# Performance work log

Measured on AMD Instinct MI355X. Metric: run time of the kernel, lower is better.

The kernel has to match this reference:

```python
import jax, jax.numpy as jnp
import numpy as np

EMBED_DIM = 2048
NUM_HEADS = 16
HEAD_DIM = EMBED_DIM // NUM_HEADS  # 128
GROUP = 256
NEG = -1e9


def setup_inputs() -> dict:
    key = jax.random.key(0)
    ks = jax.random.split(key, 4)
    B, N, C = 2, 8192, EMBED_DIM
    s = 1.0 / np.sqrt(C).astype(np.float32)
    return {
        "x": jax.random.normal(ks[0], (B, N, C), jnp.float32),
        "Wq": jax.random.normal(ks[1], (C, C), jnp.float32) * s,
        "bq": jnp.zeros((C,), jnp.float32),
        "Wk": jax.random.normal(ks[2], (C, C), jnp.float32) * s,
        "bk": jnp.zeros((C,), jnp.float32),
        "Wv": jax.random.normal(ks[3], (C, C), jnp.float32) * s,
        "bv": jnp.zeros((C,), jnp.float32),
    }


def _s2_attn(x, Wq, bq, Wk, bk, Wv, bv):
    B, N, C = x.shape
    H, hd, gs = NUM_HEADS, HEAD_DIM, GROUP
    G = N // gs
    half = H // 2

    def heads(t):  # [B,N,C] -> [B,H,N,hd]
        return t.reshape(B, N, H, hd).transpose(0, 2, 1, 3)

    q = heads(x @ Wq.T + bq)
    k = heads(x @ Wk.T + bk)
    v = heads(x @ Wv.T + bv)

    def shift(t, s):  # shift second half of heads along sequence
        return jnp.concatenate([t[:, :half], jnp.roll(t[:, half:], s, axis=2)], axis=1)

    q, k, v = shift(q, -(gs // 2)), shift(k, -(gs // 2)), shift(v, -(gs // 2))

    # group-local attention: [B,H,G,gs,hd]
    qg = q.reshape(B, H, G, gs, hd)
    kg = k.reshape(B, H, G, gs, hd)
    vg = v.reshape(B, H, G, gs, hd)

    scores = jnp.einsum("bhgqd,bhgkd->bhgqk", qg, kg) / np.sqrt(hd).astype(x.dtype)
    causal = jnp.triu(jnp.ones((gs, gs), bool), 1)  # mask strictly-upper triangle
    scores = jnp.where(causal, NEG, scores)
    attn = jax.nn.softmax(scores, axis=-1)
    out = jnp.einsum("bhgqk,bhgkd->bhgqd", attn, vg).reshape(B, H, N, hd)

    out = shift(out, gs // 2)  # un-shift the shifted heads
    return out.transpose(0, 2, 1, 3).reshape(B, N, C)


def reference(x, Wq, bq, Wk, bk, Wv, bv):
    return _s2_attn(x, Wq, bq, Wk, bk, Wv, bv)
```

## Files before the change

kernel.cpp:

```cpp
#include <hip/hip_runtime.h>
#include <hip/hip_bf16.h>

#define NSEQ 8192
#define CDIM 2048
#define NHEAD 16
#define HD 128

typedef short short8 __attribute__((ext_vector_type(8)));
typedef short short4v __attribute__((ext_vector_type(4)));
typedef float float4v __attribute__((ext_vector_type(4)));

__device__ __forceinline__ short f2bf(float f) {
    __hip_bfloat16 h = __float2bfloat16(f);
    return *reinterpret_cast<short*>(&h);
}

__device__ __forceinline__ void async_load16(const short* g, short* l) {
    __builtin_amdgcn_global_load_lds((const __attribute__((address_space(1))) void*)g,
                                     (__attribute__((address_space(3))) void*)l,
                                     16, 0, 0);
}

#define X8 (33554432 / 8)
#define W8 (4194304 / 8)

__global__ __launch_bounds__(256) void cvt_all(
    const float* __restrict__ x, const float* __restrict__ wq,
    const float* __restrict__ wk, const float* __restrict__ wv,
    short* __restrict__ xb, short* __restrict__ wqb,
    short* __restrict__ wkb, short* __restrict__ wvb)
{
    const size_t i = (size_t)blockIdx.x * blockDim.x + threadIdx.x;
    const float* src;
    short* dst;
    size_t off;
    if (i < X8)              { src = x;  dst = xb;  off = i; }
    else if (i < X8 + W8)    { src = wq; dst = wqb; off = i - X8; }
    else if (i < X8 + 2*W8)  { src = wk; dst = wkb; off = i - X8 - W8; }
    else                     { src = wv; dst = wvb; off = i - X8 - 2*(size_t)W8; }
    const float4v a = ((const float4v*)src)[off * 2];
    const float4v b = ((const float4v*)src)[off * 2 + 1];
    short8 o;
    for (int j = 0; j < 4; j++) { o[j] = f2bf(a[j]); o[4 + j] = f2bf(b[j]); }
    ((short8*)dst)[off] = o;
}

#define PBAR()  asm volatile("s_barrier" ::: "memory")
#define LGKM0() do { asm volatile("s_waitcnt lgkmcnt(0)" ::: "memory"); \
                     __builtin_amdgcn_sched_barrier(0); } while (0)
#define VMC4()  asm volatile("s_waitcnt vmcnt(4)" ::: "memory")
#define VMC0()  asm volatile("s_waitcnt vmcnt(0)" ::: "memory")

#define MFMA(d, x, y) d = __builtin_amdgcn_mfma_f32_16x16x32_bf16(x, y, d, 0, 0, 0)

__global__ __launch_bounds__(512, 2) void qkv_gemm8(
    const short* __restrict__ xb,
    const short* __restrict__ W, const float* __restrict__ bias,
    float* __restrict__ qout, short* __restrict__ kt, short* __restrict__ vt,
    const int mat)
{
    __shared__ short lds[2][2][256 * 64];

    const int tid  = threadIdx.x;
    const int w    = tid >> 6;
    const int lane = tid & 63;
    const int quad = lane >> 4;
    const int l15  = lane & 15;
    const int wm   = w >> 2;
    const int wn   = w & 3;

    const int id    = (blockIdx.x & 7) * 64 + (blockIdx.x >> 3);
    const int mtile = id >> 3;
    const int ntile = id & 7;
    const int M0 = mtile << 8;
    const int N0 = ntile << 8;

    const short* Ab = xb + (size_t)M0 * CDIM;
    const short* Bb = W  + (size_t)N0 * CDIM;

    const int stg_row = tid >> 3;
    const int stg_col = ((tid & 7) * 8) ^ (((tid >> 3) & 7) << 3);
    const int cswz    = (lane & 7) << 3;

    float bvals[4];
#pragma unroll
    for (int j = 0; j < 4; ++j)
        bvals[j] = bias[N0 + wn * 64 + j * 16 + l15];
    VMC0();

    float4v acc[8][4];
#pragma unroll
    for (int i = 0; i < 8; ++i)
#pragma unroll
        for (int j = 0; j < 4; ++j)
            acc[i][j] = (float4v){0.f, 0.f, 0.f, 0.f};

    auto stage = [&](int bufi, int ab, int h, int t, const short* src) {
        short* l0 = &lds[bufi][ab][h * 8192 + w * 512];
        const short* g = src + (size_t)(h * 128 + stg_row) * CDIM + t * 64 + stg_col;
        async_load16(g, l0);
        async_load16(g + (size_t)64 * CDIM, l0 + 4096);
    };
    auto ldA = [&](int bufi, int i, int ks) -> short8 {
        const int row = wm * 128 + i * 16 + l15;
        return *(const short8*)&lds[bufi][0][row * 64 + ((ks * 32 + quad * 8) ^ cswz)];
    };
    auto ldB = [&](int bufi, int j, int ks) -> short8 {
        const int row = wn * 64 + j * 16 + l15;
        return *(const short8*)&lds[bufi][1][row * 64 + ((ks * 32 + quad * 8) ^ cswz)];
    };

    stage(0, 0, 0, 0, Ab); stage(0, 0, 1, 0, Ab);
    stage(0, 1, 0, 0, Bb); stage(0, 1, 1, 0, Bb);
    stage(1, 1, 0, 1, Bb); stage(1, 1, 1, 1, Bb);
    VMC4();
    PBAR();

    short8 a[4][2], b[4][2];
    for (int it = 0; it < 16; ++it) {
        const int t1 = 2 * it + 1;
        const int t2 = (2 * it + 2 > 31) ? 31 : 2 * it + 2;
        const int t3 = (2 * it + 3 > 31) ? 31 : 2 * it + 3;

#pragma unroll
        for (int i = 0; i < 4; ++i) { a[i][0] = ldA(0, i, 0); a[i][1] = ldA(0, i, 1); }
#pragma unroll
        for (int j = 0; j < 2; ++j) { b[j][0] = ldB(0, j, 0); b[j][1] = ldB(0, j, 1); }
        stage(1, 0, 0, t1, Ab); stage(1, 0, 1, t1, Ab);
        PBAR(); LGKM0();
        __builtin_amdgcn_s_setprio(1);
#pragma unroll
        for (int i = 0; i < 4; ++i)
#pragma unroll
            for (int j = 0; j < 2; ++j) { MFMA(acc[i][j], a[i][0], b[j][0]);
                                          MFMA(acc[i][j], a[i][1], b[j][1]); }
        __builtin_amdgcn_s_setprio(0);
        PBAR();

#pragma unroll
        for (int j = 2; j < 4; ++j) { b[j][0] = ldB(0, j, 0); b[j][1] = ldB(0, j, 1); }
        PBAR(); LGKM0();
        __builtin_amdgcn_s_setprio(1);
#pragma unroll
        for (int i = 0; i < 4; ++i)
#pragma unroll
            for (int j = 2; j < 4; ++j) { MFMA(acc[i][j], a[i][0], b[j][0]);
                                          MFMA(acc[i][j], a[i][1], b[j][1]); }
        __builtin_amdgcn_s_setprio(0);
        PBAR();

#pragma unroll
        for (int i = 0; i < 4; ++i) { a[i][0] = ldA(0, 4 + i, 0); a[i][1] = ldA(0, 4 + i, 1); }
        stage(0, 1, 0, t2, Bb);
        PBAR(); LGKM0();
        __builtin_amdgcn_s_setprio(1);
#pragma unroll
        for (int i = 0; i < 4; ++i)
#pragma unroll
            for (int j = 2; j < 4; ++j) { MFMA(acc[4 + i][j], a[i][0], b[j][0]);
                                          MFMA(acc[4 + i][j], a[i][1], b[j][1]); }
        __builtin_amdgcn_s_setprio(0);
        PBAR();

        stage(0, 1, 1, t2, Bb);
        PBAR(); LGKM0();
        __builtin_amdgcn_s_setprio(1);
#pragma unroll
        for (int i = 0; i < 4; ++i)
#pragma unroll
            for (int j = 0; j < 2; ++j) { MFMA(acc[4 + i][j], a[i][0], b[j][0]);
                                          MFMA(acc[4 + i][j], a[i][1], b[j][1]); }
        __builtin_amdgcn_s_setprio(0);
        VMC4();
        PBAR();

#pragma unroll
        for (int i = 0; i < 4; ++i) { a[i][0] = ldA(1, i, 0); a[i][1] = ldA(1, i, 1); }
#pragma unroll
        for (int j = 0; j < 2; ++j) { b[j][0] = ldB(1, j, 0); b[j][1] = ldB(1, j, 1); }
        stage(0, 0, 0, t2, Ab); stage(0, 0, 1, t2, Ab);
        PBAR(); LGKM0();
        __builtin_amdgcn_s_setprio(1);
#pragma unroll
        for (int i = 0; i < 4; ++i)
#pragma unroll
            for (int j = 0; j < 2; ++j) { MFMA(acc[i][j], a[i][0], b[j][0]);
                                          MFMA(acc[i][j], a[i][1], b[j][1]); }
        __builtin_amdgcn_s_setprio(0);
        PBAR();

#pragma unroll
        for (int j = 2; j < 4; ++j) { b[j][0] = ldB(1, j, 0); b[j][1] = ldB(1, j, 1); }
        PBAR(); LGKM0();
        __builtin_amdgcn_s_setprio(1);
#pragma unroll
        for (int i = 0; i < 4; ++i)
#pragma unroll
            for (int j = 2; j < 4; ++j) { MFMA(acc[i][j], a[i][0], b[j][0]);
                                          MFMA(acc[i][j], a[i][1], b[j][1]); }
        __builtin_amdgcn_s_setprio(0);
        PBAR();

#pragma unroll
        for (int i = 0; i < 4; ++i) { a[i][0] = ldA(1, 4 + i, 0); a[i][1] = ldA(1, 4 + i, 1); }
        stage(1, 1, 0, t3, Bb);
        PBAR(); LGKM0();
        __builtin_amdgcn_s_setprio(1);
#pragma unroll
        for (int i = 0; i < 4; ++i)
#pragma unroll
            for (int j = 2; j < 4; ++j) { MFMA(acc[4 + i][j], a[i][0], b[j][0]);
                                          MFMA(acc[4 + i][j], a[i][1], b[j][1]); }
        __builtin_amdgcn_s_setprio(0);
        PBAR();

        stage(1, 1, 1, t3, Bb);
        PBAR(); LGKM0();
        __builtin_amdgcn_s_setprio(1);
#pragma unroll
        for (int i = 0; i < 4; ++i)
#pragma unroll
            for (int j = 0; j < 2; ++j) { MFMA(acc[4 + i][j], a[i][0], b[j][0]);
                                          MFMA(acc[4 + i][j], a[i][1], b[j][1]); }
        __builtin_amdgcn_s_setprio(0);
        VMC4();
        PBAR();
    }

#pragma unroll
    for (int j = 0; j < 4; ++j) {
        const int n = N0 + wn * 64 + j * 16 + l15;
        if (mat == 0) {
#pragma unroll
            for (int i = 0; i < 8; ++i) {
                const int mrow = M0 + wm * 128 + i * 16 + quad * 4;
#pragma unroll
                for (int r = 0; r < 4; ++r)
                    qout[((size_t)(mrow + r) << 11) + n] = acc[i][j][r] + bvals[j];
            }
        } else if (mat == 1) {
            const int h = n >> 7;
            const int d = n & (HD - 1);
#pragma unroll
            for (int i = 0; i < 8; ++i) {
                const int mrow = M0 + wm * 128 + i * 16 + quad * 4;
#pragma unroll
                for (int r = 0; r < 4; ++r) {
                    const int m  = mrow + r;
                    const int bb = m >> 13;
                    const int sq = m & (NSEQ - 1);
                    kt[(((size_t)(bb * NHEAD + h) * NSEQ + sq) << 7) + d] =
                        f2bf(acc[i][j][r] + bvals[j]);
                }
            }
        } else {
            const int h = n >> 7;
            const int d = n & (HD - 1);
#pragma unroll
            for (int i = 0; i < 8; ++i) {
                const int mrow = M0 + wm * 128 + i * 16 + quad * 4;
                const int bb = mrow >> 13;
                const int sq = mrow & (NSEQ - 1);
                short4v o4;
#pragma unroll
                for (int r = 0; r < 4; ++r) o4[r] = f2bf(acc[i][j][r] + bvals[j]);
                *(short4v*)&vt[(((size_t)(bb * NHEAD + h) * HD + d) << 13) + sq] = o4;
            }
        }
    }
}

__global__ __launch_bounds__(512, 1) void s2_attn(const float* qsrc,
                                                  const short* __restrict__ kt,
                                                  const short* __restrict__ vt,
                                                  float* out)
{
    __shared__ short Ks[64 * 136];
    __shared__ short Vt[2][128 * 64];
    __shared__ short Ps[8][32 * 40];

    const int bx = blockIdx.x;
    const int g  = bx & 31;
    const int h  = (bx >> 5) & 15;
    const int b  = bx >> 9;
    const int shift = (h >= 8) ? 128 : 0;
    const int sbase = g * 256 + shift;

    const int tid  = threadIdx.x;
    const int wave = tid >> 6;
    const int lane = tid & 63;
    const int quad = lane >> 4;
    const int l15  = lane & 15;

    const size_t bh = ((size_t)b * NHEAD + h) * NSEQ;
    const short* kg = kt + bh * HD;
    const short* vg = vt + bh * HD;

    const int mtA = wave;
    const int mtB = wave + 8;

    const int vrow_in_w = lane >> 3;
    const int vgcol     = ((lane & 7) * 8) ^ (vrow_in_w << 3);
    const int krow0 = tid >> 4;
    const int kcolb = (tid & 15) * 8;

    short8 kr0, kr1;

    {
        const int p = (sbase + vgcol) & (NSEQ - 1);
#pragma unroll
        for (int c = 0; c < 2; c++) {
            const int d = c * 64 + wave * 8 + vrow_in_w;
            async_load16(vg + (size_t)d * NSEQ + p, &Vt[0][(c * 64 + wave * 8) * 64]);
        }
        const int p0 = (sbase + krow0) & (NSEQ - 1);
        const int p1 = (sbase + krow0 + 32) & (NSEQ - 1);
        kr0 = *(const short8*)(kg + (size_t)p0 * HD + kcolb);
        kr1 = *(const short8*)(kg + (size_t)p1 * HD + kcolb);
    }

    short8 qf[2][4];
#pragma unroll
    for (int im = 0; im < 2; im++) {
        const int mt  = im ? mtB : mtA;
        const int row = mt * 16 + l15;
        const int p   = (sbase + row) & (NSEQ - 1);
        const float* qr = qsrc + (((size_t)(b * NSEQ + p)) << 11) + h * HD;
#pragma unroll
        for (int ks = 0; ks < 4; ks++) {
            const float4v qa = *(const float4v*)(qr + ks * 32 + quad * 8);
            const float4v qb = *(const float4v*)(qr + ks * 32 + quad * 8 + 4);
            short8 f;
#pragma unroll
            for (int j = 0; j < 4; j++) { f[j] = f2bf(qa[j]); f[4 + j] = f2bf(qb[j]); }
            qf[im][ks] = f;
        }
    }

    const float4v fzero = {0.f, 0.f, 0.f, 0.f};
    float4v o[2][8];
#pragma unroll
    for (int im = 0; im < 2; im++)
#pragma unroll
        for (int dt = 0; dt < 8; dt++)
            o[im][dt] = fzero;
    float rs[2][4] = {{0.f, 0.f, 0.f, 0.f}, {0.f, 0.f, 0.f, 0.f}};

    for (int kc = 0; kc < 4; kc++) {
        VMC0();
        *(short8*)&Ks[krow0 * 136 + kcolb]        = kr0;
        *(short8*)&Ks[(krow0 + 32) * 136 + kcolb] = kr1;
        LGKM0();
        PBAR();

        if (kc < 3) {
            const int p = (sbase + (kc + 1) * 64 + vgcol) & (NSEQ - 1);
#pragma unroll
            for (int c = 0; c < 2; c++) {
                const int d = c * 64 + wave * 8 + vrow_in_w;
                async_load16(vg + (size_t)d * NSEQ + p,
                             &Vt[(kc + 1) & 1][(c * 64 + wave * 8) * 64]);
            }
            const int p0 = (sbase + (kc + 1) * 64 + krow0) & (NSEQ - 1);
            const int p1 = (sbase + (kc + 1) * 64 + krow0 + 32) & (NSEQ - 1);
            kr0 = *(const short8*)(kg + (size_t)p0 * HD + kcolb);
            kr1 = *(const short8*)(kg + (size_t)p1 * HD + kcolb);
        }

        const bool hA[2] = {(4 * kc)     <= mtA, (4 * kc + 2) <= mtA};
        const bool hB[2] = {(4 * kc)     <= mtB, (4 * kc + 2) <= mtB};

        float4v s[2][4];
#pragma unroll
        for (int im = 0; im < 2; im++)
#pragma unroll
            for (int nn = 0; nn < 4; nn++)
                s[im][nn] = fzero;
        __builtin_amdgcn_s_setprio(1);
#pragma unroll
        for (int nn = 0; nn < 4; nn++) {
            const int hh = nn >> 1;
            if (hB[hh]) {
                short8 kf[4];
#pragma unroll
                for (int ks = 0; ks < 4; ks++)
                    kf[ks] = *(const short8*)&Ks[(nn * 16 + l15) * 136 + ks * 32 + quad * 8];
                if (hA[hh]) {
#pragma unroll
                    for (int ks = 0; ks < 4; ks++)
                        s[0][nn] = __builtin_amdgcn_mfma_f32_16x16x32_bf16(
                            qf[0][ks], kf[ks], s[0][nn], 0, 0, 0);
                }
#pragma unroll
                for (int ks = 0; ks < 4; ks++)
                    s[1][nn] = __builtin_amdgcn_mfma_f32_16x16x32_bf16(
                        qf[1][ks], kf[ks], s[1][nn], 0, 0, 0);
            }
        }
        __builtin_amdgcn_s_setprio(0);

#pragma unroll
        for (int half = 0; half < 2; half++) {
            if (!hB[half]) continue;
#pragma unroll
            for (int im = 0; im < 2; im++) {
                if (im == 0 && !hA[half]) continue;
                const int mt   = im ? mtB : mtA;
                const int qpos = mt * 16 + quad * 4;
#pragma unroll
                for (int nn2 = 0; nn2 < 2; nn2++) {
                    const int nn   = half * 2 + nn2;
                    const int kpos = kc * 64 + nn * 16 + l15;
#pragma unroll
                    for (int r = 0; r < 4; r++) {
                        const float sv = s[im][nn][r] * 0.088388347648318447f;
                        const float pv = (kpos > qpos + r)
                                             ? 0.f
                                             : __expf(fminf(sv, 30.f));
                        rs[im][r] += pv;
                        Ps[wave][(im * 16 + quad * 4 + r) * 40 + nn2 * 16 + l15] = f2bf(pv);
                    }
                }
            }
            LGKM0();
            short8 pf[2];
            if (hA[half])
                pf[0] = *(const short8*)&Ps[wave][(0 * 16 + l15) * 40 + quad * 8];
            pf[1] = *(const short8*)&Ps[wave][(1 * 16 + l15) * 40 + quad * 8];
            __builtin_amdgcn_s_setprio(1);
#pragma unroll
            for (int dt = 0; dt < 8; dt++) {
                const int d = dt * 16 + l15;
                const short8 vf = *(const short8*)
                    &Vt[kc & 1][d * 64 + ((half * 32 + quad * 8) ^ ((l15 & 7) << 3))];
                if (hA[half])
                    o[0][dt] = __builtin_amdgcn_mfma_f32_16x16x32_bf16(
                        pf[0], vf, o[0][dt], 0, 0, 0);
                o[1][dt] = __builtin_amdgcn_mfma_f32_16x16x32_bf16(
                    pf[1], vf, o[1][dt], 0, 0, 0);
            }
            __builtin_amdgcn_s_setprio(0);
        }
        PBAR();
    }

#pragma unroll
    for (int im = 0; im < 2; im++)
#pragma unroll
        for (int r = 0; r < 4; r++) {
            float v = rs[im][r];
            v += __shfl_xor(v, 1);
            v += __shfl_xor(v, 2);
            v += __shfl_xor(v, 4);
            v += __shfl_xor(v, 8);
            rs[im][r] = v;
        }

#pragma unroll
    for (int im = 0; im < 2; im++) {
        const int mt = im ? mtB : mtA;
#pragma unroll
        for (int r = 0; r < 4; r++) {
            const int row = mt * 16 + quad * 4 + r;
            const int p   = (sbase + row) & (NSEQ - 1);
            const float inv = 1.f / rs[im][r];
            const size_t obase = (((size_t)(b * NSEQ + p)) << 11) + h * HD;
#pragma unroll
            for (int dt = 0; dt < 8; dt++)
                out[obase + dt * 16 + l15] = o[im][dt][r] * inv;
        }
    }
}

extern "C" void kernel_launch(void* const* d_in, const int* in_sizes, int n_in,
                              void* d_out, int out_size, void* d_ws, size_t ws_size,
                              hipStream_t stream) {
    (void)in_sizes; (void)n_in; (void)out_size; (void)ws_size;
    const float* x  = (const float*)d_in[0];
    const float* Wq = (const float*)d_in[1];
    const float* bq = (const float*)d_in[2];
    const float* Wk = (const float*)d_in[3];
    const float* bk = (const float*)d_in[4];
    const float* Wv = (const float*)d_in[5];
    const float* bv = (const float*)d_in[6];

    short* xb  = (short*)d_ws;
    short* wqb = xb  + (size_t)33554432;
    short* wkb = wqb + (size_t)4194304;
    short* wvb = wkb + (size_t)4194304;
    short* kt  = wvb + (size_t)4194304;
    short* vt  = kt  + (size_t)33554432;

    float* outp = (float*)d_out;

    cvt_all<<<dim3(22528), 256, 0, stream>>>(x, Wq, Wk, Wv, xb, wqb, wkb, wvb);
    qkv_gemm8<<<dim3(512), 512, 0, stream>>>(xb, wqb, bq, outp, kt, vt, 0);
    qkv_gemm8<<<dim3(512), 512, 0, stream>>>(xb, wkb, bk, outp, kt, vt, 1);
    qkv_gemm8<<<dim3(512), 512, 0, stream>>>(xb, wvb, bv, outp, kt, vt, 2);
    s2_attn<<<dim3(1024), 512, 0, stream>>>(outp, kt, vt, outp);
}
```

Baseline: 746.6 us.

## Merge Q/K/V GEMM launches into one grid and grid-stride the conversion kernel

The three separate QKV projection GEMM launches become a single 1536-block launch. Each block picks its matrix (Q, K or V) from the block index, with a swizzle that groups the three projections of the same x row tile together to improve L2 reuse of x. This removes two kernel launch gaps and the tail imbalance between them. The fp32-to-bf16 conversion kernel now uses a grid-stride loop with 16 elements per thread and a smaller grid, which cuts block scheduling overhead.

```diff
diff --git a/kernel.cpp b/kernel.cpp
--- a/kernel.cpp
+++ b/kernel.cpp
@@ -21,8 +21,9 @@
                                      16, 0, 0);
 }
 
-#define X8 (33554432 / 8)
-#define W8 (4194304 / 8)
+#define X16 (33554432 / 16)
+#define W16 (4194304 / 16)
+#define TOT16 (X16 + 3 * W16)
 
 __global__ __launch_bounds__(256) void cvt_all(
     const float* __restrict__ x, const float* __restrict__ wq,
@@ -30,19 +31,30 @@
     short* __restrict__ xb, short* __restrict__ wqb,
     short* __restrict__ wkb, short* __restrict__ wvb)
 {
-    const size_t i = (size_t)blockIdx.x * blockDim.x + threadIdx.x;
-    const float* src;
-    short* dst;
-    size_t off;
-    if (i < X8)              { src = x;  dst = xb;  off = i; }
-    else if (i < X8 + W8)    { src = wq; dst = wqb; off = i - X8; }
-    else if (i < X8 + 2*W8)  { src = wk; dst = wkb; off = i - X8 - W8; }
-    else                     { src = wv; dst = wvb; off = i - X8 - 2*(size_t)W8; }
-    const float4v a = ((const float4v*)src)[off * 2];
-    const float4v b = ((const float4v*)src)[off * 2 + 1];
-    short8 o;
-    for (int j = 0; j < 4; j++) { o[j] = f2bf(a[j]); o[4 + j] = f2bf(b[j]); }
-    ((short8*)dst)[off] = o;
+    const size_t stride = (size_t)gridDim.x * blockDim.x;
+    for (size_t i = (size_t)blockIdx.x * blockDim.x + threadIdx.x;
+         i < (size_t)TOT16; i += stride) {
+        const float* src;
+        short* dst;
+        size_t off;
+        if (i < X16)                 { src = x;  dst = xb;  off = i; }
+        else if (i < X16 + W16)      { src = wq; dst = wqb; off = i - X16; }
+        else if (i < X16 + 2 * W16)  { src = wk; dst = wkb; off = i - X16 - W16; }
+        else                         { src = wv; dst = wvb; off = i - X16 - 2 * (size_t)W16; }
+        const float4v* s4 = (const float4v*)src + off * 4;
+        const float4v a0 = s4[0], a1 = s4[1], a2 = s4[2], a3 = s4[3];
+        short8 o0, o1;
+#pragma unroll
+        for (int j = 0; j < 4; j++) {
+            o0[j]     = f2bf(a0[j]);
+            o0[4 + j] = f2bf(a1[j]);
+            o1[j]     = f2bf(a2[j]);
+            o1[4 + j] = f2bf(a3[j]);
+        }
+        short8* d8 = (short8*)dst + off * 2;
+        d8[0] = o0;
+        d8[1] = o1;
+    }
 }
 
 #define PBAR()  asm volatile("s_barrier" ::: "memory")
@@ -55,9 +67,10 @@
 
 __global__ __launch_bounds__(512, 2) void qkv_gemm8(
     const short* __restrict__ xb,
-    const short* __restrict__ W, const float* __restrict__ bias,
-    float* __restrict__ qout, short* __restrict__ kt, short* __restrict__ vt,
-    const int mat)
+    const short* __restrict__ Wq, const float* __restrict__ bq,
+    const short* __restrict__ Wk, const float* __restrict__ bk,
+    const short* __restrict__ Wv, const float* __restrict__ bv,
+    float* __restrict__ qout, short* __restrict__ kt, short* __restrict__ vt)
 {
     __shared__ short lds[2][2][256 * 64];
 
@@ -69,12 +82,16 @@
     const int wm   = w >> 2;
     const int wn   = w & 3;
 
-    const int id    = (blockIdx.x & 7) * 64 + (blockIdx.x >> 3);
-    const int mtile = id >> 3;
-    const int ntile = id & 7;
+    const int id    = (blockIdx.x & 7) * 192 + (blockIdx.x >> 3);
+    const int mtile = id / 24;
+    const int rest  = id - mtile * 24;
+    const int mat   = rest >> 3;
+    const int ntile = rest & 7;
     const int M0 = mtile << 8;
     const int N0 = ntile << 8;
 
+    const short* W    = (mat == 0) ? Wq : (mat == 1) ? Wk : Wv;
+    const float* bias = (mat == 0) ? bq : (mat == 1) ? bk : bv;
     const short* Ab = xb + (size_t)M0 * CDIM;
     const short* Bb = W  + (size_t)N0 * CDIM;
 
@@ -493,9 +510,8 @@
 
     float* outp = (float*)d_out;
 
-    cvt_all<<<dim3(22528), 256, 0, stream>>>(x, Wq, Wk, Wv, xb, wqb, wkb, wvb);
-    qkv_gemm8<<<dim3(512), 512, 0, stream>>>(xb, wqb, bq, outp, kt, vt, 0);
-    qkv_gemm8<<<dim3(512), 512, 0, stream>>>(xb, wkb, bk, outp, kt, vt, 1);
-    qkv_gemm8<<<dim3(512), 512, 0, stream>>>(xb, wvb, bv, outp, kt, vt, 2);
+    cvt_all<<<dim3(2048), 256, 0, stream>>>(x, Wq, Wk, Wv, xb, wqb, wkb, wvb);
+    qkv_gemm8<<<dim3(1536), 512, 0, stream>>>(xb, wqb, bq, wkb, bk, wvb, bv,
+                                              outp, kt, vt);
     s2_attn<<<dim3(1024), 512, 0, stream>>>(outp, kt, vt, outp);
 }
```

After: 726.5 us. -2.7%, faster.

## Merge Q/K/V GEMMs into one persistent kernel with next-tile prefetch

Applied to the files above, without the earlier changes.

Replaces three separate GEMM launches of 512 blocks with one launch of 256 persistent blocks. Each block works through 6 output tiles drawn from the Q, K and V matrices, ordered so tiles that share the same x rows stay on the same XCD. While the epilogue stores the current tile, the block already issues async LDS loads for the next tile, which hides pipeline fill and removes two launch gaps. The trade-off is one resident block per CU instead of two, which lowers the wave-level latency hiding within the main loop.

```diff
diff --git a/kernel.cpp b/kernel.cpp
--- a/kernel.cpp
+++ b/kernel.cpp
@@ -55,9 +55,10 @@
 
 __global__ __launch_bounds__(512, 2) void qkv_gemm8(
     const short* __restrict__ xb,
-    const short* __restrict__ W, const float* __restrict__ bias,
-    float* __restrict__ qout, short* __restrict__ kt, short* __restrict__ vt,
-    const int mat)
+    const short* __restrict__ Wq, const float* __restrict__ bq,
+    const short* __restrict__ Wk, const float* __restrict__ bk,
+    const short* __restrict__ Wv, const float* __restrict__ bv,
+    float* __restrict__ qout, short* __restrict__ kt, short* __restrict__ vt)
 {
     __shared__ short lds[2][2][256 * 64];
 
@@ -69,31 +70,27 @@
     const int wm   = w >> 2;
     const int wn   = w & 3;
 
-    const int id    = (blockIdx.x & 7) * 64 + (blockIdx.x >> 3);
-    const int mtile = id >> 3;
-    const int ntile = id & 7;
-    const int M0 = mtile << 8;
-    const int N0 = ntile << 8;
-
-    const short* Ab = xb + (size_t)M0 * CDIM;
-    const short* Bb = W  + (size_t)N0 * CDIM;
+    const int xcd = blockIdx.x & 7;
+    const int c   = blockIdx.x >> 3;
 
     const int stg_row = tid >> 3;
     const int stg_col = ((tid & 7) * 8) ^ (((tid >> 3) & 7) << 3);
     const int cswz    = (lane & 7) << 3;
 
-    float bvals[4];
-#pragma unroll
-    for (int j = 0; j < 4; ++j)
-        bvals[j] = bias[N0 + wn * 64 + j * 16 + l15];
-    VMC0();
-
-    float4v acc[8][4];
-#pragma unroll
-    for (int i = 0; i < 8; ++i)
-#pragma unroll
-        for (int j = 0; j < 4; ++j)
-            acc[i][j] = (float4v){0.f, 0.f, 0.f, 0.f};
+    auto decode = [&](int a, int& mat, int& M0, int& N0,
+                      const short*& Ab, const short*& Bb, const float*& bias) {
+        const int id    = xcd * 192 + c * 6 + a;
+        const int mtile = id / 24;
+        const int rest  = id - mtile * 24;
+        mat = rest >> 3;
+        const int ntile = rest & 7;
+        M0 = mtile << 8;
+        N0 = ntile << 8;
+        const short* W = (mat == 0) ? Wq : (mat == 1) ? Wk : Wv;
+        bias = (mat == 0) ? bq : (mat == 1) ? bk : bv;
+        Ab = xb + (size_t)M0 * CDIM;
+        Bb = W  + (size_t)N0 * CDIM;
+    };
 
     auto stage = [&](int bufi, int ab, int h, int t, const short* src) {
         short* l0 = &lds[bufi][ab][h * 8192 + w * 512];
@@ -110,162 +107,203 @@
         return *(const short8*)&lds[bufi][1][row * 64 + ((ks * 32 + quad * 8) ^ cswz)];
     };
 
+    int mat, M0, N0;
+    const short *Ab, *Bb;
+    const float* bias;
+    decode(0, mat, M0, N0, Ab, Bb, bias);
+
+    float bvals[4];
+#pragma unroll
+    for (int j = 0; j < 4; ++j)
+        bvals[j] = bias[N0 + wn * 64 + j * 16 + l15];
+
     stage(0, 0, 0, 0, Ab); stage(0, 0, 1, 0, Ab);
     stage(0, 1, 0, 0, Bb); stage(0, 1, 1, 0, Bb);
     stage(1, 1, 0, 1, Bb); stage(1, 1, 1, 1, Bb);
     VMC4();
     PBAR();
 
+    float4v acc[8][4];
     short8 a[4][2], b[4][2];
-    for (int it = 0; it < 16; ++it) {
-        const int t1 = 2 * it + 1;
-        const int t2 = (2 * it + 2 > 31) ? 31 : 2 * it + 2;
-        const int t3 = (2 * it + 3 > 31) ? 31 : 2 * it + 3;
-
-#pragma unroll
-        for (int i = 0; i < 4; ++i) { a[i][0] = ldA(0, i, 0); a[i][1] = ldA(0, i, 1); }
-#pragma unroll
-        for (int j = 0; j < 2; ++j) { b[j][0] = ldB(0, j, 0); b[j][1] = ldB(0, j, 1); }
-        stage(1, 0, 0, t1, Ab); stage(1, 0, 1, t1, Ab);
-        PBAR(); LGKM0();
-        __builtin_amdgcn_s_setprio(1);
-#pragma unroll
-        for (int i = 0; i < 4; ++i)
-#pragma unroll
-            for (int j = 0; j < 2; ++j) { MFMA(acc[i][j], a[i][0], b[j][0]);
-                                          MFMA(acc[i][j], a[i][1], b[j][1]); }
-        __builtin_amdgcn_s_setprio(0);
-        PBAR();
-
-#pragma unroll
-        for (int j = 2; j < 4; ++j) { b[j][0] = ldB(0, j, 0); b[j][1] = ldB(0, j, 1); }
-        PBAR(); LGKM0();
-        __builtin_amdgcn_s_setprio(1);
-#pragma unroll
-        for (int i = 0; i < 4; ++i)
-#pragma unroll
-            for (int j = 2; j < 4; ++j) { MFMA(acc[i][j], a[i][0], b[j][0]);
-                                          MFMA(acc[i][j], a[i][1], b[j][1]); }
-        __builtin_amdgcn_s_setprio(0);
-        PBAR();
-
-#pragma unroll
-        for (int i = 0; i < 4; ++i) { a[i][0] = ldA(0, 4 + i, 0); a[i][1] = ldA(0, 4 + i, 1); }
-        stage(0, 1, 0, t2, Bb);
-        PBAR(); LGKM0();
-        __builtin_amdgcn_s_setprio(1);
-#pragma unroll
-        for (int i = 0; i < 4; ++i)
-#pragma unroll
-            for (int j = 2; j < 4; ++j) { MFMA(acc[4 + i][j], a[i][0], b[j][0]);
-                                          MFMA(acc[4 + i][j], a[i][1], b[j][1]); }
-        __builtin_amdgcn_s_setprio(0);
-        PBAR();
-
-        stage(0, 1, 1, t2, Bb);
-        PBAR(); LGKM0();
-        __builtin_amdgcn_s_setprio(1);
-#pragma unroll
-        for (int i = 0; i < 4; ++i)
-#pragma unroll
-            for (int j = 0; j < 2; ++j) { MFMA(acc[4 + i][j], a[i][0], b[j][0]);
-                                          MFMA(acc[4 + i][j], a[i][1], b[j][1]); }
-        __builtin_amdgcn_s_setprio(0);
-        VMC4();
-        PBAR();
-
-#pragma unroll
-        for (int i = 0; i < 4; ++i) { a[i][0] = ldA(1, i, 0); a[i][1] = ldA(1, i, 1); }
-#pragma unroll
-        for (int j = 0; j < 2; ++j) { b[j][0] = ldB(1, j, 0); b[j][1] = ldB(1, j, 1); }
-        stage(0, 0, 0, t2, Ab); stage(0, 0, 1, t2, Ab);
-        PBAR(); LGKM0();
-        __builtin_amdgcn_s_setprio(1);
-#pragma unroll
-        for (int i = 0; i < 4; ++i)
-#pragma unroll
-            for (int j = 0; j < 2; ++j) { MFMA(acc[i][j], a[i][0], b[j][0]);
-                                          MFMA(acc[i][j], a[i][1], b[j][1]); }
-        __builtin_amdgcn_s_setprio(0);
-        PBAR();
-
-#pragma unroll
-        for (int j = 2; j < 4; ++j) { b[j][0] = ldB(1, j, 0); b[j][1] = ldB(1, j, 1); }
-        PBAR(); LGKM0();
-        __builtin_amdgcn_s_setprio(1);
-#pragma unroll
-        for (int i = 0; i < 4; ++i)
-#pragma unroll
-            for (int j = 2; j < 4; ++j) { MFMA(acc[i][j], a[i][0], b[j][0]);
-                                          MFMA(acc[i][j], a[i][1], b[j][1]); }
-        __builtin_amdgcn_s_setprio(0);
-        PBAR();
-
-#pragma unroll
-        for (int i = 0; i < 4; ++i) { a[i][0] = ldA(1, 4 + i, 0); a[i][1] = ldA(1, 4 + i, 1); }
-        stage(1, 1, 0, t3, Bb);
-        PBAR(); LGKM0();
-        __builtin_amdgcn_s_setprio(1);
-#pragma unroll
-        for (int i = 0; i < 4; ++i)
-#pragma unroll
-            for (int j = 2; j < 4; ++j) { MFMA(acc[4 + i][j], a[i][0], b[j][0]);
-                                          MFMA(acc[4 + i][j], a[i][1], b[j][1]); }
-        __builtin_amdgcn_s_setprio(0);
-        PBAR();
-
-        stage(1, 1, 1, t3, Bb);
-        PBAR(); LGKM0();
-        __builtin_amdgcn_s_setprio(1);
-#pragma unroll
-        for (int i = 0; i < 4; ++i)
-#pragma unroll
-            for (int j = 0; j < 2; ++j) { MFMA(acc[4 + i][j], a[i][0], b[j][0]);
-                                          MFMA(acc[4 + i][j], a[i][1], b[j][1]); }
-        __builtin_amdgcn_s_setprio(0);
-        VMC4();
-        PBAR();
-    }
-
-#pragma unroll
-    for (int j = 0; j < 4; ++j) {
-        const int n = N0 + wn * 64 + j * 16 + l15;
-        if (mat == 0) {
-#pragma unroll
-            for (int i = 0; i < 8; ++i) {
-                const int mrow = M0 + wm * 128 + i * 16 + quad * 4;
-#pragma unroll
-                for (int r = 0; r < 4; ++r)
-                    qout[((size_t)(mrow + r) << 11) + n] = acc[i][j][r] + bvals[j];
-            }
-        } else if (mat == 1) {
-            const int h = n >> 7;
-            const int d = n & (HD - 1);
-#pragma unroll
-            for (int i = 0; i < 8; ++i) {
-                const int mrow = M0 + wm * 128 + i * 16 + quad * 4;
-#pragma unroll
-                for (int r = 0; r < 4; ++r) {
-                    const int m  = mrow + r;
-                    const int bb = m >> 13;
-                    const int sq = m & (NSEQ - 1);
-                    kt[(((size_t)(bb * NHEAD + h) * NSEQ + sq) << 7) + d] =
-                        f2bf(acc[i][j][r] + bvals[j]);
+
+    for (int asg = 0; asg < 6; ++asg) {
+#pragma unroll
+        for (int i = 0; i < 8; ++i)
+#pragma unroll
+            for (int j = 0; j < 4; ++j)
+                acc[i][j] = (float4v){0.f, 0.f, 0.f, 0.f};
+
+        for (int it = 0; it < 16; ++it) {
+            const int t1 = 2 * it + 1;
+            const int t2 = (2 * it + 2 > 31) ? 31 : 2 * it + 2;
+            const int t3 = (2 * it + 3 > 31) ? 31 : 2 * it + 3;
+
+#pragma unroll
+            for (int i = 0; i < 4; ++i) { a[i][0] = ldA(0, i, 0); a[i][1] = ldA(0, i, 1); }
+#pragma unroll
+            for (int j = 0; j < 2; ++j) { b[j][0] = ldB(0, j, 0); b[j][1] = ldB(0, j, 1); }
+            stage(1, 0, 0, t1, Ab); stage(1, 0, 1, t1, Ab);
+            PBAR(); LGKM0();
+            __builtin_amdgcn_s_setprio(1);
+#pragma unroll
+            for (int i = 0; i < 4; ++i)
+#pragma unroll
+                for (int j = 0; j < 2; ++j) { MFMA(acc[i][j], a[i][0], b[j][0]);
+                                              MFMA(acc[i][j], a[i][1], b[j][1]); }
+            __builtin_amdgcn_s_setprio(0);
+            PBAR();
+
+#pragma unroll
+            for (int j = 2; j < 4; ++j) { b[j][0] = ldB(0, j, 0); b[j][1] = ldB(0, j, 1); }
+            PBAR(); LGKM0();
+            __builtin_amdgcn_s_setprio(1);
+#pragma unroll
+            for (int i = 0; i < 4; ++i)
+#pragma unroll
+                for (int j = 2; j < 4; ++j) { MFMA(acc[i][j], a[i][0], b[j][0]);
+                                              MFMA(acc[i][j], a[i][1], b[j][1]); }
+            __builtin_amdgcn_s_setprio(0);
+            PBAR();
+
+#pragma unroll
+            for (int i = 0; i < 4; ++i) { a[i][0] = ldA(0, 4 + i, 0); a[i][1] = ldA(0, 4 + i, 1); }
+            stage(0, 1, 0, t2, Bb);
+            PBAR(); LGKM0();
+            __builtin_amdgcn_s_setprio(1);
+#pragma unroll
+            for (int i = 0; i < 4; ++i)
+#pragma unroll
+                for (int j = 2; j < 4; ++j) { MFMA(acc[4 + i][j], a[i][0], b[j][0]);
+                                              MFMA(acc[4 + i][j], a[i][1], b[j][1]); }
+            __builtin_amdgcn_s_setprio(0);
+            PBAR();
+
+            stage(0, 1, 1, t2, Bb);
+            PBAR(); LGKM0();
+            __builtin_amdgcn_s_setprio(1);
+#pragma unroll
+            for (int i = 0; i < 4; ++i)
+#pragma unroll
+                for (int j = 0; j < 2; ++j) { MFMA(acc[4 + i][j], a[i][0], b[j][0]);
+                                              MFMA(acc[4 + i][j], a[i][1], b[j][1]); }
+            __builtin_amdgcn_s_setprio(0);
+            VMC4();
+            PBAR();
+
+#pragma unroll
+            for (int i = 0; i < 4; ++i) { a[i][0] = ldA(1, i, 0); a[i][1] = ldA(1, i, 1); }
+#pragma unroll
+            for (int j = 0; j < 2; ++j) { b[j][0] = ldB(1, j, 0); b[j][1] = ldB(1, j, 1); }
+            stage(0, 0, 0, t2, Ab); stage(0, 0, 1, t2, Ab);
+            PBAR(); LGKM0();
+            __builtin_amdgcn_s_setprio(1);
+#pragma unroll
+            for (int i = 0; i < 4; ++i)
+#pragma unroll
+                for (int j = 0; j < 2; ++j) { MFMA(acc[i][j], a[i][0], b[j][0]);
+                                              MFMA(acc[i][j], a[i][1], b[j][1]); }
+            __builtin_amdgcn_s_setprio(0);
+            PBAR();
+
+#pragma unroll
+            for (int j = 2; j < 4; ++j) { b[j][0] = ldB(1, j, 0); b[j][1] = ldB(1, j, 1); }
+            PBAR(); LGKM0();
+            __builtin_amdgcn_s_setprio(1);
+#pragma unroll
+            for (int i = 0; i < 4; ++i)
+#pragma unroll
+                for (int j = 2; j < 4; ++j) { MFMA(acc[i][j], a[i][0], b[j][0]);
+                                              MFMA(acc[i][j], a[i][1], b[j][1]); }
+            __builtin_amdgcn_s_setprio(0);
+            PBAR();
+
+#pragma unroll
+            for (int i = 0; i < 4; ++i) { a[i][0] = ldA(1, 4 + i, 0); a[i][1] = ldA(1, 4 + i, 1); }
+            stage(1, 1, 0, t3, Bb);
+            PBAR(); LGKM0();
+            __builtin_amdgcn_s_setprio(1);
+#pragma unroll
+            for (int i = 0; i < 4; ++i)
+#pragma unroll
+                for (int j = 2; j < 4; ++j) { MFMA(acc[4 + i][j], a[i][0], b[j][0]);
+                                              MFMA(acc[4 + i][j], a[i][1], b[j][1]); }
+            __builtin_amdgcn_s_setprio(0);
+            PBAR();
+
+            stage(1, 1, 1, t3, Bb);
+            PBAR(); LGKM0();
+            __builtin_amdgcn_s_setprio(1);
+#pragma unroll
+            for (int i = 0; i < 4; ++i)
+#pragma unroll
+                for (int j = 0; j < 2; ++j) { MFMA(acc[4 + i][j], a[i][0], b[j][0]);
+                                              MFMA(acc[4 + i][j], a[i][1], b[j][1]); }
+            __builtin_amdgcn_s_setprio(0);
+            VMC4();
+            PBAR();
+        }
+
+        const int mat_c = mat, M0_c = M0, N0_c = N0;
+        float bv_c[4];
+#pragma unroll
+        for (int j = 0; j < 4; ++j) bv_c[j] = bvals[j];
+
+        if (asg < 5) {
+            VMC0();
+            decode(asg + 1, mat, M0, N0, Ab, Bb, bias);
+#pragma unroll
+            for (int j = 0; j < 4; ++j)
+                bvals[j] = bias[N0 + wn * 64 + j * 16 + l15];
+            stage(0, 0, 0, 0, Ab); stage(0, 0, 1, 0, Ab);
+            stage(0, 1, 0, 0, Bb); stage(0, 1, 1, 0, Bb);
+            stage(1, 1, 0, 1, Bb); stage(1, 1, 1, 1, Bb);
+        }
+
+#pragma unroll
+        for (int j = 0; j < 4; ++j) {
+            const int n = N0_c + wn * 64 + j * 16 + l15;
+            if (mat_c == 0) {
+#pragma unroll
+                for (int i = 0; i < 8; ++i) {
+                    const int mrow = M0_c + wm * 128 + i * 16 + quad * 4;
+#pragma unroll
+                    for (int r = 0; r < 4; ++r)
+                        qout[((size_t)(mrow + r) << 11) + n] = acc[i][j][r] + bv_c[j];
+                }
+            } else if (mat_c == 1) {
+                const int h = n >> 7;
+                const int d = n & (HD - 1);
+#pragma unroll
+                for (int i = 0; i < 8; ++i) {
+                    const int mrow = M0_c + wm * 128 + i * 16 + quad * 4;
+#pragma unroll
+                    for (int r = 0; r < 4; ++r) {
+                        const int m  = mrow + r;
+                        const int bb = m >> 13;
+                        const int sq = m & (NSEQ - 1);
+                        kt[(((size_t)(bb * NHEAD + h) * NSEQ + sq) << 7) + d] =
+                            f2bf(acc[i][j][r] + bv_c[j]);
+                    }
+                }
+            } else {
+                const int h = n >> 7;
+                const int d = n & (HD - 1);
+#pragma unroll
+                for (int i = 0; i < 8; ++i) {
+                    const int mrow = M0_c + wm * 128 + i * 16 + quad * 4;
+                    const int bb = mrow >> 13;
+                    const int sq = mrow & (NSEQ - 1);
+                    short4v o4;
+#pragma unroll
+                    for (int r = 0; r < 4; ++r) o4[r] = f2bf(acc[i][j][r] + bv_c[j]);
+                    *(short4v*)&vt[(((size_t)(bb * NHEAD + h) * HD + d) << 13) + sq] = o4;
                 }
             }
-        } else {
-            const int h = n >> 7;
-            const int d = n & (HD - 1);
-#pragma unroll
-            for (int i = 0; i < 8; ++i) {
-                const int mrow = M0 + wm * 128 + i * 16 + quad * 4;
-                const int bb = mrow >> 13;
-                const int sq = mrow & (NSEQ - 1);
-                short4v o4;
-#pragma unroll
-                for (int r = 0; r < 4; ++r) o4[r] = f2bf(acc[i][j][r] + bvals[j]);
-                *(short4v*)&vt[(((size_t)(bb * NHEAD + h) * HD + d) << 13) + sq] = o4;
-            }
+        }
+
+        if (asg < 5) {
+            VMC4();
+            PBAR();
         }
     }
 }
@@ -494,8 +532,7 @@
     float* outp = (float*)d_out;
 
     cvt_all<<<dim3(22528), 256, 0, stream>>>(x, Wq, Wk, Wv, xb, wqb, wkb, wvb);
-    qkv_gemm8<<<dim3(512), 512, 0, stream>>>(xb, wqb, bq, outp, kt, vt, 0);
-    qkv_gemm8<<<dim3(512), 512, 0, stream>>>(xb, wkb, bk, outp, kt, vt, 1);
-    qkv_gemm8<<<dim3(512), 512, 0, stream>>>(xb, wvb, bv, outp, kt, vt, 2);
+    qkv_gemm8<<<dim3(256), 512, 0, stream>>>(xb, wqb, bq, wkb, bk, wvb, bv,
+                                             outp, kt, vt);
     s2_attn<<<dim3(1024), 512, 0, stream>>>(outp, kt, vt, outp);
 }
```

Result: slower. 772.2 us (+3.4%).
